# Optimization experiments

Hardware: AMD Instinct MI355X
Metric: run time of the kernel (lower is better)

## Reference

```python
import jax, jax.numpy as jnp
import numpy as np

U1, U2 = 128, 32  # GRU units


def gru(x, kernel, rec_kernel, bias, act, rec_act):
    """Keras GRU with reset_after=True. x: [B,T,F], kernel: [F,3U],
    rec_kernel: [U,3U], bias: [2,3U] (input bias, recurrent bias).
    Gate order is [z, r, h]. Returns (sequence [B,T,U], last state [B,U])."""
    B = x.shape[0]
    U = rec_kernel.shape[0]
    # Precompute the input projection for all timesteps in one big matmul.
    xb = jnp.einsum('btf,fg->btg', x, kernel) + bias[0]  # [B,T,3U]

    def step(h, xt):
        inner = h @ rec_kernel + bias[1]                 # [B,3U]
        xz, xr, xh = jnp.split(xt, 3, axis=-1)
        iz, ir, ih = jnp.split(inner, 3, axis=-1)
        z = rec_act(xz + iz)
        r = rec_act(xr + ir)
        hh = act(xh + r * ih)
        h_new = z * h + (1.0 - z) * hh
        return h_new, h_new

    h0 = jnp.zeros((B, U), x.dtype)
    hT, hs = jax.lax.scan(step, h0, jnp.swapaxes(xb, 0, 1))  # scan over T
    return jnp.swapaxes(hs, 0, 1), hT


def setup_inputs() -> dict:
    key = jax.random.key(0)
    ks = jax.random.split(key, 9)
    B, T, F = 512, 1024, 1
    s = 0.05
    return {
        'x':   jax.random.normal(ks[0], (B, T, F), jnp.float32),
        'k1':  jax.random.normal(ks[1], (F, 3 * U1), jnp.float32) * s,
        'rk1': jax.random.normal(ks[2], (U1, 3 * U1), jnp.float32) * s,
        'b1':  jnp.zeros((2, 3 * U1), jnp.float32),
        'k2':  jax.random.normal(ks[3], (U1, 3 * U2), jnp.float32) * s,
        'rk2': jax.random.normal(ks[4], (U2, 3 * U2), jnp.float32) * s,
        'b2':  jnp.zeros((2, 3 * U2), jnp.float32),
        'wd':  jax.random.normal(ks[5], (U2, 1), jnp.float32) * s,
        'bd':  jnp.zeros((1,), jnp.float32),
    }


def reference(x, k1, rk1, b1, k2, rk2, b2, wd, bd):
    # GRU-1: activation=tanh, recurrent_activation=relu, return_sequences=True
    seq1, _ = gru(x, k1, rk1, b1, jnp.tanh, jax.nn.relu)
    # Dropout(0.5) is identity at inference time.
    # GRU-2: activation=relu, recurrent_activation=sigmoid, return last state
    _, h2 = gru(seq1, k2, rk2, b2, jax.nn.relu, jax.nn.sigmoid)
    return h2 @ wd + bd  # [B,1]
```

## Files before the change

kernel.cpp:

```cpp
#include <hip/hip_runtime.h>
#include <math.h>

#define TT 1024
#define U1 128
#define U2 32
#define NCOL 480
#define NCP 240
#define NUQ 4

typedef float f2 __attribute__((ext_vector_type(2)));

#define PK_LO(acc, w, h) asm("v_pk_fma_f32 %0, %1, %2, %0 op_sel:[0,0,0] op_sel_hi:[1,0,1]" \
                             : "+v"(acc) : "v"(w), "v"(h))
#define PK_HI(acc, w, h) asm("v_pk_fma_f32 %0, %1, %2, %0 op_sel:[0,1,0] op_sel_hi:[1,1,1]" \
                             : "+v"(acc) : "v"(w), "v"(h))

__device__ __forceinline__ float fast_tanh(float v) {
    float e = __expf(2.f * v);
    return 1.f - 2.f / (e + 1.f);
}
__device__ __forceinline__ float fast_sig(float v) {
    return 1.f / (1.f + __expf(-v));
}

__global__ __launch_bounds__(1024, 2)
void gru_stack_kernel(const float* __restrict__ x,
                      const float* __restrict__ k1,
                      const float* __restrict__ rk1,
                      const float* __restrict__ b1,
                      const float* __restrict__ k2,
                      const float* __restrict__ rk2,
                      const float* __restrict__ b2,
                      const float* __restrict__ wd,
                      const float* __restrict__ bd,
                      float* __restrict__ out)
{
    __shared__ __align__(16) float h1s[U1];
    __shared__ __align__(16) float h2s[U2];
    __shared__ __align__(16) float part1[NUQ][NCOL];
    __shared__ __align__(16) float part2[96];
    __shared__ __align__(16) float xs[TT];

    const int t = threadIdx.x;
    const int b = blockIdx.x;

    if (t < U1) h1s[t] = 0.f;
    if (t < U2) h2s[t] = 0.f;
    if (t < TT) xs[t] = x[b * TT + t];

    f2 w2[32];
    const float4* pb = nullptr;
    float2* pd = nullptr;
    const bool is_dot = (t < 1008);
    if (t < 960) {
        const int uq = t / NCP, p = t % NCP;
        const int c0 = 2 * p, ub = 32 * uq;
#pragma unroll
        for (int j = 0; j < 32; ++j) {
            const int u = ub + j;
            float vv[2];
#pragma unroll
            for (int r = 0; r < 2; ++r) {
                const int c = c0 + r;
                vv[r] = (c < 384) ? rk1[u * 384 + c] : k2[u * 96 + (c - 384)];
            }
            w2[j].x = vv[0]; w2[j].y = vv[1];
        }
        pb = (const float4*)&h1s[ub];
        pd = (float2*)&part1[uq][c0];
    } else if (t < 1008) {
        const int q2 = t - 960, c0 = 2 * q2;
#pragma unroll
        for (int j = 0; j < 32; ++j) {
            w2[j].x = rk2[j * 96 + c0 + 0];
            w2[j].y = rk2[j * 96 + c0 + 1];
        }
        pb = (const float4*)&h2s[0];
        pd = (float2*)&part2[c0];
    } else {
#pragma unroll
        for (int j = 0; j < 32; ++j) { w2[j].x = 0.f; w2[j].y = 0.f; }
    }

    const int ju = t;
    float k1z = 0, k1r = 0, k1h = 0, bz = 0, br = 0, bhx = 0, bhr = 0, h_old = 0;
    if (t < 128) {
        k1z = k1[ju]; k1r = k1[128 + ju]; k1h = k1[256 + ju];
        bz  = b1[ju]       + b1[384 + ju];
        br  = b1[128 + ju] + b1[384 + 128 + ju];
        bhx = b1[256 + ju];
        bhr = b1[384 + 256 + ju];
    }
    const int j2 = t - 128;
    float bz2 = 0, br2 = 0, bh2x = 0, bh2r = 0, h2_old = 0;
    if (t >= 128 && t < 160) {
        bz2  = b2[j2]      + b2[96 + j2];
        br2  = b2[32 + j2] + b2[96 + 32 + j2];
        bh2x = b2[64 + j2];
        bh2r = b2[96 + 64 + j2];
    }

    __syncthreads();

    for (int i = 0; i <= TT; ++i) {
        if (is_dot) {
            f2 a = {0.f, 0.f};
#pragma unroll
            for (int k = 0; k < 8; ++k) {
                const float4 h4 = pb[k];
                const f2 hlo = {h4.x, h4.y}, hhi = {h4.z, h4.w};
                PK_LO(a, w2[4 * k],     hlo);
                PK_HI(a, w2[4 * k + 1], hlo);
                PK_LO(a, w2[4 * k + 2], hhi);
                PK_HI(a, w2[4 * k + 3], hhi);
            }
            *pd = make_float2(a.x, a.y);
        }
        __syncthreads();

        if (t < 128 && i < TT) {
            const float xv = xs[i];
            float iz = part1[0][ju] + part1[1][ju]
                     + part1[2][ju] + part1[3][ju];
            float ir = part1[0][128 + ju] + part1[1][128 + ju]
                     + part1[2][128 + ju] + part1[3][128 + ju];
            float ih = part1[0][256 + ju] + part1[1][256 + ju]
                     + part1[2][256 + ju] + part1[3][256 + ju];
            float z  = fmaxf(fmaf(xv, k1z, bz) + iz, 0.f);
            float r  = fmaxf(fmaf(xv, k1r, br) + ir, 0.f);
            float hh = fast_tanh(fmaf(xv, k1h, bhx) + r * (ih + bhr));
            h_old = fmaf(z, h_old - hh, hh);
            h1s[ju] = h_old;
        } else if (t >= 128 && t < 160 && i >= 1) {
            float xz = part1[0][384 + j2] + part1[1][384 + j2]
                     + part1[2][384 + j2] + part1[3][384 + j2];
            float xr = part1[0][416 + j2] + part1[1][416 + j2]
                     + part1[2][416 + j2] + part1[3][416 + j2];
            float xh = part1[0][448 + j2] + part1[1][448 + j2]
                     + part1[2][448 + j2] + part1[3][448 + j2];
            float iz = part2[j2];
            float ir = part2[32 + j2];
            float ih = part2[64 + j2];
            float z  = fast_sig(xz + iz + bz2);
            float r  = fast_sig(xr + ir + br2);
            float hh = fmaxf(xh + bh2x + r * (ih + bh2r), 0.f);
            h2_old = fmaf(z, h2_old - hh, hh);
            h2s[j2] = h2_old;
        }
        __syncthreads();
    }

    if (t < 32) {
        float p = h2s[t] * wd[t];
#pragma unroll
        for (int m = 16; m >= 1; m >>= 1) p += __shfl_xor(p, m, 64);
        if (t == 0) out[b] = p + bd[0];
    }
}

extern "C" void kernel_launch(void* const* d_in, const int* in_sizes, int n_in,
                              void* d_out, int out_size, void* d_ws, size_t ws_size,
                              hipStream_t stream) {
    const float* x   = (const float*)d_in[0];
    const float* k1  = (const float*)d_in[1];
    const float* rk1 = (const float*)d_in[2];
    const float* b1  = (const float*)d_in[3];
    const float* k2  = (const float*)d_in[4];
    const float* rk2 = (const float*)d_in[5];
    const float* b2  = (const float*)d_in[6];
    const float* wd  = (const float*)d_in[7];
    const float* bd  = (const float*)d_in[8];
    float* out = (float*)d_out;

    dim3 grid(512), block(1024);
    hipLaunchKernelGGL(gru_stack_kernel, grid, block, 0, stream,
                       x, k1, rk1, b1, k2, rk2, b2, wd, bd, out);
}
```

Measured before the change: 1.369 ms.

## Process two batch rows per block with shuffle reductions and one barrier per step

Each block now handles two sequences, so every register-resident weight is reused for both rows' dot products. Partial sums are reduced with cross-lane shuffles instead of a shared partial array, and hidden states are double-buffered by step parity. This cuts the per-step barriers from two to one and pipelines layer 2 one step behind layer 1. In exchange the grid halves to 256 blocks, leaving fewer blocks to spread across the GPU's compute units, and the lane mapping becomes more intricate.

Measured after the change: 1.954 ms. 42.8% more time.

```diff
diff --git a/kernel.cpp b/kernel.cpp
--- a/kernel.cpp
+++ b/kernel.cpp
@@ -4,11 +4,9 @@
 #define TT 1024
 #define U1 128
 #define U2 32
-#define NCOL 480
-#define NCP 240
-#define NUQ 4
 
 typedef float f2 __attribute__((ext_vector_type(2)));
+typedef float f4 __attribute__((ext_vector_type(4)));
 
 #define PK_LO(acc, w, h) asm("v_pk_fma_f32 %0, %1, %2, %0 op_sel:[0,0,0] op_sel_hi:[1,0,1]" \
                              : "+v"(acc) : "v"(w), "v"(h))
@@ -23,7 +21,7 @@
     return 1.f / (1.f + __expf(-v));
 }
 
-__global__ __launch_bounds__(1024, 2)
+__global__ __launch_bounds__(1024)
 void gru_stack_kernel(const float* __restrict__ x,
                       const float* __restrict__ k1,
                       const float* __restrict__ rk1,
@@ -35,126 +33,158 @@
                       const float* __restrict__ bd,
                       float* __restrict__ out)
 {
-    __shared__ __align__(16) float h1s[U1];
-    __shared__ __align__(16) float h2s[U2];
-    __shared__ __align__(16) float part1[NUQ][NCOL];
-    __shared__ __align__(16) float part2[96];
-    __shared__ __align__(16) float xs[TT];
-
-    const int t = threadIdx.x;
-    const int b = blockIdx.x;
-
-    if (t < U1) h1s[t] = 0.f;
-    if (t < U2) h2s[t] = 0.f;
-    if (t < TT) xs[t] = x[b * TT + t];
+    __shared__ __align__(16) float h1p[2][2][4][36];
+    __shared__ __align__(16) f2    h2b[2][U2];
+    __shared__ __align__(16) float k2g[2][2][96];
+    __shared__ __align__(16) f2    xs2[TT];
+
+    const int t    = threadIdx.x;
+    const int b0   = blockIdx.x * 2;
+    const int oct  = t >> 3, ol = t & 7;
+    const int pr   = ol >> 2;
+    const int uq   = ol & 3, ub = 32 * uq;
+    const int U    = oct;
+    const int lane = t & 63, qb = lane & ~3;
+    const int r2   = U - 96;
+
+    if (t < 576) ((float*)h1p)[t] = 0.f;
+    if (t < 64)  ((f2*)h2b)[t] = (f2){0.f, 0.f};
+    if (t < 384) ((float*)k2g)[t] = 0.f;
+    if (t < TT)  xs2[t] = (f2){ x[b0 * TT + t], x[(b0 + 1) * TT + t] };
 
     f2 w2[32];
-    const float4* pb = nullptr;
-    float2* pd = nullptr;
-    const bool is_dot = (t < 1008);
-    if (t < 960) {
-        const int uq = t / NCP, p = t % NCP;
-        const int c0 = 2 * p, ub = 32 * uq;
-#pragma unroll
-        for (int j = 0; j < 32; ++j) {
-            const int u = ub + j;
-            float vv[2];
-#pragma unroll
-            for (int r = 0; r < 2; ++r) {
-                const int c = c0 + r;
-                vv[r] = (c < 384) ? rk1[u * 384 + c] : k2[u * 96 + (c - 384)];
-            }
-            w2[j].x = vv[0]; w2[j].y = vv[1];
-        }
-        pb = (const float4*)&h1s[ub];
-        pd = (float2*)&part1[uq][c0];
-    } else if (t < 1008) {
-        const int q2 = t - 960, c0 = 2 * q2;
-#pragma unroll
-        for (int j = 0; j < 32; ++j) {
-            w2[j].x = rk2[j * 96 + c0 + 0];
-            w2[j].y = rk2[j * 96 + c0 + 1];
-        }
-        pb = (const float4*)&h2s[0];
-        pd = (float2*)&part2[c0];
-    } else {
-#pragma unroll
-        for (int j = 0; j < 32; ++j) { w2[j].x = 0.f; w2[j].y = 0.f; }
-    }
-
-    const int ju = t;
-    float k1z = 0, k1r = 0, k1h = 0, bz = 0, br = 0, bhx = 0, bhr = 0, h_old = 0;
-    if (t < 128) {
-        k1z = k1[ju]; k1r = k1[128 + ju]; k1h = k1[256 + ju];
-        bz  = b1[ju]       + b1[384 + ju];
-        br  = b1[128 + ju] + b1[384 + 128 + ju];
-        bhx = b1[256 + ju];
-        bhr = b1[384 + 256 + ju];
-    }
-    const int j2 = t - 128;
-    float bz2 = 0, br2 = 0, bh2x = 0, bh2r = 0, h2_old = 0;
-    if (t >= 128 && t < 160) {
-        bz2  = b2[j2]      + b2[96 + j2];
-        br2  = b2[32 + j2] + b2[96 + 32 + j2];
-        bh2x = b2[64 + j2];
-        bh2r = b2[96 + 64 + j2];
+#pragma unroll
+    for (int j = 0; j < 32; ++j) {
+        const int u = ub + j;
+        if (pr == 0) {
+            w2[j] = (f2){ rk1[u * 384 + U], rk1[u * 384 + 128 + U] };
+        } else {
+            float c1w;
+            if (U < 96)       c1w = k2[u * 96 + U];
+            else if (uq < 3)  c1w = rk2[j * 96 + 32 * uq + r2];
+            else              c1w = 0.f;
+            w2[j] = (f2){ rk1[u * 384 + 256 + U], c1w };
+        }
+    }
+
+    const float k1z = k1[U], k1r = k1[128 + U], k1h = k1[256 + U];
+    const float bz  = b1[U]       + b1[384 + U];
+    const float br  = b1[128 + U] + b1[384 + 128 + U];
+    const float bhx = b1[256 + U];
+    const float bhr = b1[384 + 256 + U];
+    float h_old = 0.f;
+    float bz2 = 0, br2 = 0, bh2x = 0, bh2r = 0, h2A = 0.f, h2B = 0.f;
+    if (U >= 96 && pr == 1) {
+        bz2  = b2[r2]      + b2[96 + r2];
+        br2  = b2[32 + r2] + b2[96 + 32 + r2];
+        bh2x = b2[64 + r2];
+        bh2r = b2[96 + 64 + r2];
     }
 
     __syncthreads();
 
-    for (int i = 0; i <= TT; ++i) {
-        if (is_dot) {
-            f2 a = {0.f, 0.f};
+    for (int p = 0; p <= TT + 1; ++p) {
+        const int wpar = p & 1, rpar = wpar ^ 1;
+
+        if (p <= TT) {
+            const f4* pbA = (const f4*)&h1p[rpar][0][uq][0];
+            const f4* pbB = (const f4*)&h1p[rpar][1][uq][0];
+            f2 accA = {0.f, 0.f}, accB = {0.f, 0.f};
 #pragma unroll
             for (int k = 0; k < 8; ++k) {
-                const float4 h4 = pb[k];
-                const f2 hlo = {h4.x, h4.y}, hhi = {h4.z, h4.w};
-                PK_LO(a, w2[4 * k],     hlo);
-                PK_HI(a, w2[4 * k + 1], hlo);
-                PK_LO(a, w2[4 * k + 2], hhi);
-                PK_HI(a, w2[4 * k + 3], hhi);
-            }
-            *pd = make_float2(a.x, a.y);
+                const f4 a4 = pbA[k];
+                const f4 b4 = pbB[k];
+                const f2 alo = a4.lo, ahi = a4.hi;
+                const f2 blo = b4.lo, bhi = b4.hi;
+                PK_LO(accA, w2[4 * k],     alo);
+                PK_HI(accA, w2[4 * k + 1], alo);
+                PK_LO(accA, w2[4 * k + 2], ahi);
+                PK_HI(accA, w2[4 * k + 3], ahi);
+                PK_LO(accB, w2[4 * k],     blo);
+                PK_HI(accB, w2[4 * k + 1], blo);
+                PK_LO(accB, w2[4 * k + 2], bhi);
+                PK_HI(accB, w2[4 * k + 3], bhi);
+            }
+            f2 tA, tB;
+            tA.x = __shfl_xor(accA.x, 1, 64); tA.y = __shfl_xor(accA.y, 1, 64);
+            tB.x = __shfl_xor(accB.x, 1, 64); tB.y = __shfl_xor(accB.y, 1, 64);
+            accA += tA; accB += tB;
+            tA.x = __shfl_xor(accA.x, 2, 64); tA.y = __shfl_xor(accA.y, 2, 64);
+            tB.x = __shfl_xor(accB.x, 2, 64); tB.y = __shfl_xor(accB.y, 2, 64);
+            accA += tA; accB += tB;
+            f2 othA, othB;
+            othA.x = __shfl_xor(accA.x, 4, 64); othA.y = __shfl_xor(accA.y, 4, 64);
+            othB.x = __shfl_xor(accB.x, 4, 64); othB.y = __shfl_xor(accB.y, 4, 64);
+            const float zv = pr ? othB.x : accA.x;
+            const float rv = pr ? othB.y : accA.y;
+            const float hv = pr ? accB.x : othA.x;
+            const float kv = pr ? accB.y : othA.y;
+
+            if (p < TT) {
+                const f2 xp = xs2[p];
+                const float xv = pr ? xp.y : xp.x;
+                const float z  = fmaxf(fmaf(xv, k1z, bz) + zv, 0.f);
+                const float r  = fmaxf(fmaf(xv, k1r, br) + rv, 0.f);
+                const float hh = fast_tanh(fmaf(xv, k1h, bhx) + r * (hv + bhr));
+                h_old = fmaf(z, h_old - hh, hh);
+                if ((ol & 3) == 0)
+                    h1p[wpar][pr][U >> 5][U & 31] = h_old;
+            }
+            if ((ol & 3) == 0 && U < 96)
+                k2g[wpar][pr][U] = kv;
+        }
+
+        if (t >= 768) {
+            const f4* ph2 = (const f4*)&h2b[rpar][0];
+            f2 mAB = {0.f, 0.f};
+#pragma unroll
+            for (int k = 0; k < 16; ++k) {
+                const f4 q = ph2[k];
+                const f2 qlo = q.lo, qhi = q.hi;
+                PK_HI(mAB, qlo, w2[2 * k]);
+                PK_HI(mAB, qhi, w2[2 * k + 1]);
+            }
+            f2 g0, g1, g2;
+            g0.x = __shfl(mAB.x, qb + 0, 64); g0.y = __shfl(mAB.y, qb + 0, 64);
+            g1.x = __shfl(mAB.x, qb + 1, 64); g1.y = __shfl(mAB.y, qb + 1, 64);
+            g2.x = __shfl(mAB.x, qb + 2, 64); g2.y = __shfl(mAB.y, qb + 2, 64);
+            if (p >= 2 && pr == 1) {
+                {
+                    const float xz = k2g[rpar][0][r2];
+                    const float xr = k2g[rpar][0][32 + r2];
+                    const float xh = k2g[rpar][0][64 + r2];
+                    const float z  = fast_sig(xz + g0.x + bz2);
+                    const float rr = fast_sig(xr + g1.x + br2);
+                    const float hh = fmaxf(xh + bh2x + rr * (g2.x + bh2r), 0.f);
+                    h2A = fmaf(z, h2A - hh, hh);
+                }
+                {
+                    const float xz = k2g[rpar][1][r2];
+                    const float xr = k2g[rpar][1][32 + r2];
+                    const float xh = k2g[rpar][1][64 + r2];
+                    const float z  = fast_sig(xz + g0.y + bz2);
+                    const float rr = fast_sig(xr + g1.y + br2);
+                    const float hh = fmaxf(xh + bh2x + rr * (g2.y + bh2r), 0.f);
+                    h2B = fmaf(z, h2B - hh, hh);
+                }
+                if (uq == 0) h2b[wpar][r2] = (f2){h2A, h2B};
+            }
         }
         __syncthreads();
-
-        if (t < 128 && i < TT) {
-            const float xv = xs[i];
-            float iz = part1[0][ju] + part1[1][ju]
-                     + part1[2][ju] + part1[3][ju];
-            float ir = part1[0][128 + ju] + part1[1][128 + ju]
-                     + part1[2][128 + ju] + part1[3][128 + ju];
-            float ih = part1[0][256 + ju] + part1[1][256 + ju]
-                     + part1[2][256 + ju] + part1[3][256 + ju];
-            float z  = fmaxf(fmaf(xv, k1z, bz) + iz, 0.f);
-            float r  = fmaxf(fmaf(xv, k1r, br) + ir, 0.f);
-            float hh = fast_tanh(fmaf(xv, k1h, bhx) + r * (ih + bhr));
-            h_old = fmaf(z, h_old - hh, hh);
-            h1s[ju] = h_old;
-        } else if (t >= 128 && t < 160 && i >= 1) {
-            float xz = part1[0][384 + j2] + part1[1][384 + j2]
-                     + part1[2][384 + j2] + part1[3][384 + j2];
-            float xr = part1[0][416 + j2] + part1[1][416 + j2]
-                     + part1[2][416 + j2] + part1[3][416 + j2];
-            float xh = part1[0][448 + j2] + part1[1][448 + j2]
-                     + part1[2][448 + j2] + part1[3][448 + j2];
-            float iz = part2[j2];
-            float ir = part2[32 + j2];
-            float ih = part2[64 + j2];
-            float z  = fast_sig(xz + iz + bz2);
-            float r  = fast_sig(xr + ir + br2);
-            float hh = fmaxf(xh + bh2x + r * (ih + bh2r), 0.f);
-            h2_old = fmaf(z, h2_old - hh, hh);
-            h2s[j2] = h2_old;
-        }
-        __syncthreads();
     }
 
     if (t < 32) {
-        float p = h2s[t] * wd[t];
-#pragma unroll
-        for (int m = 16; m >= 1; m >>= 1) p += __shfl_xor(p, m, 64);
-        if (t == 0) out[b] = p + bd[0];
+        const f2 hf = h2b[1][t];
+        f2 pv = hf * wd[t];
+#pragma unroll
+        for (int m = 16; m >= 1; m >>= 1) {
+            pv.x += __shfl_xor(pv.x, m, 64);
+            pv.y += __shfl_xor(pv.y, m, 64);
+        }
+        if (t == 0) {
+            out[b0]     = pv.x + bd[0];
+            out[b0 + 1] = pv.y + bd[0];
+        }
     }
 }
 
@@ -172,7 +202,7 @@
     const float* bd  = (const float*)d_in[8];
     float* out = (float*)d_out;
 
-    dim3 grid(512), block(1024);
+    dim3 grid(256), block(1024);
     hipLaunchKernelGGL(gru_stack_kernel, grid, block, 0, stream,
                        x, k1, rk1, b1, k2, rk2, b2, wd, bd, out);
 }
```
